# Kernel optimization log

Hardware: AMD Instinct MI355X
Metric: run time of the kernel (lower is better)

The kernel has to match this reference:

```python
import math
import jax, jax.numpy as jnp
import numpy as np

B, L, DIM, H = 2, 2048, 1024, 16
D = DIM // H  # head_dim = 64
EPS = 1e-6


def setup_inputs() -> dict:
    key = jax.random.key(0)
    ks = jax.random.split(key, 5)
    s = 0.02
    return {
        "x": jax.random.normal(ks[0], (B, L, DIM), jnp.float32),
        "pe": jax.random.normal(ks[1], (B, 1, L, D // 2, 2, 2), jnp.float32),
        "w_qkv": jax.random.normal(ks[2], (DIM, 3 * DIM), jnp.float32) * s,
        "q_scale": jnp.ones((D,), jnp.float32),
        "k_scale": jnp.ones((D,), jnp.float32),
        "w_proj": jax.random.normal(ks[3], (DIM, DIM), jnp.float32) * s,
        "b_proj": jnp.zeros((DIM,), jnp.float32),
    }


def _rmsnorm(t, scale):
    # flax nnx.RMSNorm: x * rsqrt(mean(x^2) + eps) * scale, over last dim
    var = jnp.mean(jnp.square(t), axis=-1, keepdims=True)
    return t * jax.lax.rsqrt(var + EPS) * scale


def _apply_rope(t, pe):
    # t: [B,H,L,D]; pe: [B,1,L,D/2,2,2]
    t2 = t.reshape(*t.shape[:-1], D // 2, 1, 2)
    out = pe[..., 0] * t2[..., 0] + pe[..., 1] * t2[..., 1]  # [B,H,L,D/2,2]
    return out.reshape(t.shape)


def reference(x, pe, w_qkv, q_scale, k_scale, w_proj, b_proj):
    # fused QKV projection
    qkv = jnp.einsum('bld,de->ble', x, w_qkv)  # [B,L,3*DIM]
    qkv = qkv.reshape(B, L, 3, H, D).transpose(2, 0, 3, 1, 4)  # [3,B,H,L,D]
    q, k, v = qkv[0], qkv[1], qkv[2]
    # QK RMSNorm
    q = _rmsnorm(q, q_scale)
    k = _rmsnorm(k, k_scale)
    # RoPE via pe
    q = _apply_rope(q, pe)
    k = _apply_rope(k, pe)
    # scaled dot product attention
    scores = jnp.einsum('bhqd,bhkd->bhqk', q, k) / math.sqrt(D)
    attn = jax.nn.softmax(scores, axis=-1)
    o = jnp.einsum('bhqk,bhkd->bhqd', attn, v)  # [B,H,L,D]
    o = o.transpose(0, 2, 1, 3).reshape(B, L, DIM)  # B H L D -> B L (H D)
    # output projection
    return jnp.einsum('bld,de->ble', o, w_proj) + b_proj
```

## Files before the change

kernel.cpp:

```cpp
#include <hip/hip_runtime.h>
#include <math.h>

#define BB 2
#define LL 2048
#define DIMM 1024
#define HH 16
#define DD 64
#define QKV_N 3072

typedef unsigned short u16;
typedef unsigned int u32;
typedef __attribute__((ext_vector_type(8))) short short8;
typedef __attribute__((ext_vector_type(4))) float f32x4;

__device__ __forceinline__ float bf2f(u16 h) {
    unsigned u = ((unsigned)h) << 16;
    return __uint_as_float(u);
}
__device__ __forceinline__ u16 f2bf(float f) {
    unsigned u = __float_as_uint(f);
    u += 0x7fffu + ((u >> 16) & 1u);
    return (u16)(u >> 16);
}
__device__ __forceinline__ u32 pack_bf2(float lo, float hi) {
    u32 a = __float_as_uint(hi) + 0x8000u;
    u32 b = __float_as_uint(lo) + 0x8000u;
    return __builtin_amdgcn_perm(a, b, 0x07060302u);
}
__device__ __forceinline__ void gload16(const u16* g, u16* l) {
    __builtin_amdgcn_global_load_lds(
        (const __attribute__((address_space(1))) void*)g,
        (__attribute__((address_space(3))) void*)l, 16, 0, 0);
}

__global__ __launch_bounds__(256) void convx(
    const float* __restrict__ X, u16* __restrict__ Xb)
{
    int i = (blockIdx.x * 256 + threadIdx.x) * 8;
    float4 a = *(const float4*)&X[i];
    float4 b = *(const float4*)&X[i + 4];
    u16 t[8] = {f2bf(a.x), f2bf(a.y), f2bf(a.z), f2bf(a.w),
                f2bf(b.x), f2bf(b.y), f2bf(b.z), f2bf(b.w)};
    *(uint4*)&Xb[i] = *(uint4*)t;
}

__global__ __launch_bounds__(256) void convt(
    const float* __restrict__ W, u16* __restrict__ Wt, int K, int N)
{
    __shared__ u16 s[64][72];
    const int tid = threadIdx.x;
    const int k0 = blockIdx.x * 64, n0 = blockIdx.y * 64;
#pragma unroll
    for (int t = 0; t < 16; ++t) {
        int flat = t * 256 + tid;
        int kk = flat >> 6, nn = flat & 63;
        s[nn][kk] = f2bf(W[(size_t)(k0 + kk) * N + n0 + nn]);
    }
    __syncthreads();
#pragma unroll
    for (int t = 0; t < 2; ++t) {
        int chunk = t * 256 + tid;
        int nn = chunk >> 3, kc = chunk & 7;
        *(uint4*)&Wt[(size_t)(n0 + nn) * K + k0 + kc * 8] = *(uint4*)&s[nn][kc * 8];
    }
}

__global__ __launch_bounds__(256) void gemm_qkv(
    const u16* __restrict__ A, const u16* __restrict__ Bt,
    u16* __restrict__ C, u16* __restrict__ vt, const float* __restrict__ pe,
    const float* __restrict__ qs, const float* __restrict__ ks)
{
    __shared__ u16 smem[2 * 128 * 64];
    u16* sA = smem;
    u16* sB = smem + 128 * 64;

    const int tid = threadIdx.x;
    const int wave = tid >> 6, lane = tid & 63;
    const int mIdx = lane & 15, quad = lane >> 4;
    const int wr = wave >> 1, wc = wave & 1;
    const int m0 = blockIdx.y * 128, n0 = blockIdx.x * 128;
    const int N = QKV_N, K = DIMM;
    const int lr = lane >> 3, lc = lane & 7;

    f32x4 acc[4][4];
#pragma unroll
    for (int a = 0; a < 4; ++a)
#pragma unroll
        for (int b = 0; b < 4; ++b) acc[a][b] = (f32x4){0.f, 0.f, 0.f, 0.f};

    for (int k0 = 0; k0 < K; k0 += 64) {
#pragma unroll
        for (int j = 0; j < 4; ++j) {
            int r0 = 32 * wave + 8 * j + lr;
            int kc = 8 * (lc ^ (r0 & 7));
            gload16(&A[(size_t)(m0 + r0) * K + k0 + kc], &sA[(32 * wave + 8 * j) * 64]);
            gload16(&Bt[(size_t)(n0 + r0) * K + k0 + kc], &sB[(32 * wave + 8 * j) * 64]);
        }
        __syncthreads();
#pragma unroll
        for (int ks2 = 0; ks2 < 2; ++ks2) {
            short8 af[4], bfr[4];
#pragma unroll
            for (int mt = 0; mt < 4; ++mt) {
                int Ra = 64 * wr + 16 * mt + mIdx;
                af[mt] = *(const short8*)&sA[Ra * 64 + 8 * ((ks2 * 4 + quad) ^ (Ra & 7))];
            }
#pragma unroll
            for (int nt = 0; nt < 4; ++nt) {
                int Rb = 64 * wc + 16 * nt + mIdx;
                bfr[nt] = *(const short8*)&sB[Rb * 64 + 8 * ((ks2 * 4 + quad) ^ (Rb & 7))];
            }
#pragma unroll
            for (int mt = 0; mt < 4; ++mt)
#pragma unroll
                for (int nt = 0; nt < 4; ++nt)
                    acc[mt][nt] = __builtin_amdgcn_mfma_f32_16x16x32_bf16(
                        af[mt], bfr[nt], acc[mt][nt], 0, 0, 0);
        }
        __syncthreads();
    }

    if (n0 >= 2048) {
#pragma unroll
        for (int mt = 0; mt < 4; ++mt) {
            int lofs = 64 * wr + 16 * mt + 4 * quad;
#pragma unroll
            for (int nt = 0; nt < 4; ++nt) {
                int d = 64 * wc + 16 * nt + mIdx;
                uint2 pr;
                pr.x = pack_bf2(acc[mt][nt][0], acc[mt][nt][1]);
                pr.y = pack_bf2(acc[mt][nt][2], acc[mt][nt][3]);
                *(uint2*)&smem[d * 128 + (lofs ^ (8 * (d & 7)))] = pr;
            }
        }
        __syncthreads();
        {
            const int d = tid >> 1, half = tid & 1;
            const int hd = n0 - 2048 + d;
            const int h = hd >> 6, dd = hd & 63;
            const int b = m0 >> 11, l0 = m0 & 2047;
            u16* dst = vt + ((size_t)((b * 16 + h) * 64 + dd)) * LL + l0 + half * 64;
#pragma unroll
            for (int c = 0; c < 8; ++c) {
                int slot = (half * 64 + 8 * c) ^ (8 * (d & 7));
                *(uint4*)&dst[8 * c] = *(const uint4*)&smem[d * 128 + slot];
            }
        }
    } else {
        const float* scv = (n0 < 1024) ? qs : ks;
        const float pre = (n0 < 1024) ? 0.18033688011112042f : 1.0f;
        float scl[4];
#pragma unroll
        for (int nt = 0; nt < 4; ++nt) scl[nt] = scv[16 * nt + mIdx];

#pragma unroll
        for (int mt = 0; mt < 4; ++mt) {
#pragma unroll
            for (int r = 0; r < 4; ++r) {
                float s = 0.f;
#pragma unroll
                for (int nt = 0; nt < 4; ++nt) {
                    float a = acc[mt][nt][r];
                    s += a * a;
                }
                s += __shfl_xor(s, 1);
                s += __shfl_xor(s, 2);
                s += __shfl_xor(s, 4);
                s += __shfl_xor(s, 8);
                float rn = rsqrtf(s * (1.f / 64.f) + 1e-6f);
                int R = m0 + 64 * wr + 16 * mt + quad * 4 + r;
                size_t peo = (size_t)R * 128;
#pragma unroll
                for (int nt = 0; nt < 4; ++nt) {
                    float v = acc[mt][nt][r] * rn * scl[nt];
                    float pp = __shfl_xor(v, 1);
                    float2 pw = *(const float2*)&pe[peo + 2 * (16 * nt + mIdx)];
                    float e  = (mIdx & 1) ? pp : v;
                    float od = (mIdx & 1) ? v : pp;
                    C[(size_t)R * N + n0 + 64 * wc + 16 * nt + mIdx] =
                        f2bf((pw.x * e + pw.y * od) * pre);
                }
            }
        }
    }
}

__global__ __launch_bounds__(256) void gemm_proj(
    const u16* __restrict__ A, const u16* __restrict__ Bt,
    const float* __restrict__ bias, float* __restrict__ C)
{
    __shared__ u16 sA[64 * 64];
    __shared__ u16 sB[128 * 64];

    const int tid = threadIdx.x;
    const int wave = tid >> 6, lane = tid & 63;
    const int mIdx = lane & 15, quad = lane >> 4;
    const int wr = wave >> 1, wc = wave & 1;
    const int m0 = blockIdx.y * 64, n0 = blockIdx.x * 128;
    const int N = DIMM, K = DIMM;
    const int lr = lane >> 3, lc = lane & 7;

    f32x4 acc[2][4];
#pragma unroll
    for (int a = 0; a < 2; ++a)
#pragma unroll
        for (int b = 0; b < 4; ++b) acc[a][b] = (f32x4){0.f, 0.f, 0.f, 0.f};

    for (int k0 = 0; k0 < K; k0 += 64) {
#pragma unroll
        for (int j = 0; j < 2; ++j) {
            int r0 = 16 * wave + 8 * j + lr;
            int kc = 8 * (lc ^ (r0 & 7));
            gload16(&A[(size_t)(m0 + r0) * K + k0 + kc], &sA[(16 * wave + 8 * j) * 64]);
        }
#pragma unroll
        for (int j = 0; j < 4; ++j) {
            int r0 = 32 * wave + 8 * j + lr;
            int kc = 8 * (lc ^ (r0 & 7));
            gload16(&Bt[(size_t)(n0 + r0) * K + k0 + kc], &sB[(32 * wave + 8 * j) * 64]);
        }
        __syncthreads();
#pragma unroll
        for (int ks2 = 0; ks2 < 2; ++ks2) {
            short8 af[2], bfr[4];
#pragma unroll
            for (int mt = 0; mt < 2; ++mt) {
                int Ra = 32 * wr + 16 * mt + mIdx;
                af[mt] = *(const short8*)&sA[Ra * 64 + 8 * ((ks2 * 4 + quad) ^ (Ra & 7))];
            }
#pragma unroll
            for (int nt = 0; nt < 4; ++nt) {
                int Rb = 64 * wc + 16 * nt + mIdx;
                bfr[nt] = *(const short8*)&sB[Rb * 64 + 8 * ((ks2 * 4 + quad) ^ (Rb & 7))];
            }
#pragma unroll
            for (int mt = 0; mt < 2; ++mt)
#pragma unroll
                for (int nt = 0; nt < 4; ++nt)
                    acc[mt][nt] = __builtin_amdgcn_mfma_f32_16x16x32_bf16(
                        af[mt], bfr[nt], acc[mt][nt], 0, 0, 0);
        }
        __syncthreads();
    }

#pragma unroll
    for (int mt = 0; mt < 2; ++mt)
#pragma unroll
        for (int r = 0; r < 4; ++r) {
            int row = m0 + 32 * wr + 16 * mt + quad * 4 + r;
#pragma unroll
            for (int nt = 0; nt < 4; ++nt) {
                int col = n0 + 64 * wc + 16 * nt + mIdx;
                C[(size_t)row * N + col] = acc[mt][nt][r] + bias[col];
            }
        }
}

#define PR 72

__global__ __launch_bounds__(512, 4) void attn_mfma(
    const u16* __restrict__ qkv, const u16* __restrict__ vt, u16* __restrict__ o)
{
    __shared__ u16 sK[2][64 * PR];
    __shared__ u16 sVt[2][64 * PR];
    __shared__ u16 sP[128 * PR];

    const int tid = threadIdx.x;
    const int wave = tid >> 6;
    const int lane = tid & 63;
    const int mIdx = lane & 15;
    const int quad = lane >> 4;

    const int bh = blockIdx.x >> 4;
    const int qt = blockIdx.x & 15;
    const int b = bh >> 4, h = bh & 15;
    const int q0 = qt * 128;

    const u16* kbase = qkv + (size_t)b * LL * QKV_N + 1024 + h * 64;
    const u16* vbase = vt + (size_t)bh * 64 * LL;

    const u16* qrow = qkv + (size_t)b * LL * QKV_N + h * 64
                      + (size_t)(q0 + 16 * wave + mIdx) * QKV_N;
    short8 aq0 = *(const short8*)&qrow[quad * 8];
    short8 aq1 = *(const short8*)&qrow[32 + quad * 8];

    const int sr = tid >> 3;
    const int sc = (tid & 7) * 8;

    {
        uint4 kv4 = *(const uint4*)&kbase[(size_t)sr * QKV_N + sc];
        uint4 vv4 = *(const uint4*)&vbase[(size_t)sr * LL + sc];
        *(uint4*)&sK[0][sr * PR + sc] = kv4;
        *(uint4*)&sVt[0][sr * PR + sc] = vv4;
    }

    float lsum = 0.f;
    f32x4 Oacc[4];
#pragma unroll
    for (int nb = 0; nb < 4; ++nb) Oacc[nb] = (f32x4){0.f, 0.f, 0.f, 0.f};

    u16* sProw = &sP[(16 * wave + mIdx) * PR];

    for (int kt = 0; kt < 32; ++kt) {
        const int p = kt & 1;
        __syncthreads();

        if (kt + 1 < 32) {
            const int k0n = (kt + 1) * 64;
            uint4 kv4 = *(const uint4*)&kbase[(size_t)(k0n + sr) * QKV_N + sc];
            uint4 vv4 = *(const uint4*)&vbase[(size_t)sr * LL + k0n + sc];
            *(uint4*)&sK[p ^ 1][sr * PR + sc] = kv4;
            *(uint4*)&sVt[p ^ 1][sr * PR + sc] = vv4;
        }

#pragma unroll
        for (int nb = 0; nb < 4; ++nb) {
            short8 bk0 = *(const short8*)&sK[p][(16 * nb + mIdx) * PR + quad * 8];
            short8 bk1 = *(const short8*)&sK[p][(16 * nb + mIdx) * PR + 32 + quad * 8];
            f32x4 st = (f32x4){0.f, 0.f, 0.f, 0.f};
            st = __builtin_amdgcn_mfma_f32_16x16x32_bf16(bk0, aq0, st, 0, 0, 0);
            st = __builtin_amdgcn_mfma_f32_16x16x32_bf16(bk1, aq1, st, 0, 0, 0);

            float p0 = exp2f(st[0]), p1 = exp2f(st[1]);
            float p2 = exp2f(st[2]), p3 = exp2f(st[3]);
            lsum += (p0 + p1) + (p2 + p3);
            u32 w0 = pack_bf2(p0, p1);
            u32 w1 = pack_bf2(p2, p3);
            uint2 wpair; wpair.x = w0; wpair.y = w1;
            *(uint2*)&sProw[16 * nb + quad * 4] = wpair;
        }

        short8 pa0 = *(const short8*)&sProw[quad * 8];
        short8 pa1 = *(const short8*)&sProw[32 + quad * 8];
#pragma unroll
        for (int nb = 0; nb < 4; ++nb) {
            short8 bv0 = *(const short8*)&sVt[p][(16 * nb + mIdx) * PR + quad * 8];
            short8 bv1 = *(const short8*)&sVt[p][(16 * nb + mIdx) * PR + 32 + quad * 8];
            Oacc[nb] = __builtin_amdgcn_mfma_f32_16x16x32_bf16(pa0, bv0, Oacc[nb], 0, 0, 0);
            Oacc[nb] = __builtin_amdgcn_mfma_f32_16x16x32_bf16(pa1, bv1, Oacc[nb], 0, 0, 0);
        }
    }

    lsum += __shfl_xor(lsum, 16);
    lsum += __shfl_xor(lsum, 32);

#pragma unroll
    for (int r = 0; r < 4; ++r) {
        float lr = __shfl(lsum, quad * 4 + r);
        float linv = 1.f / lr;
        int rowg = b * LL + q0 + 16 * wave + quad * 4 + r;
#pragma unroll
        for (int nb = 0; nb < 4; ++nb) {
            o[(size_t)rowg * DIMM + h * 64 + 16 * nb + mIdx] = f2bf(Oacc[nb][r] * linv);
        }
    }
}

extern "C" void kernel_launch(void* const* d_in, const int* in_sizes, int n_in,
                              void* d_out, int out_size, void* d_ws, size_t ws_size,
                              hipStream_t stream) {
    const float* x       = (const float*)d_in[0];
    const float* pe      = (const float*)d_in[1];
    const float* w_qkv   = (const float*)d_in[2];
    const float* q_scale = (const float*)d_in[3];
    const float* k_scale = (const float*)d_in[4];
    const float* w_proj  = (const float*)d_in[5];
    const float* b_proj  = (const float*)d_in[6];
    float* out = (float*)d_out;

    char* ws = (char*)d_ws;
    u16* qkv    = (u16*)ws;  ws += (size_t)4096 * 3072 * 2;
    u16* o      = (u16*)ws;  ws += (size_t)4096 * 1024 * 2;
    u16* xb     = (u16*)ws;  ws += (size_t)4096 * 1024 * 2;
    u16* wqkvt  = (u16*)ws;  ws += (size_t)3072 * 1024 * 2;
    u16* wprojt = (u16*)ws;  ws += (size_t)1024 * 1024 * 2;
    u16* vtbuf  = (u16*)ws;  ws += (size_t)BB * HH * DD * LL * 2;

    convx<<<(4096 * 1024) / (256 * 8), 256, 0, stream>>>(x, xb);
    convt<<<dim3(1024 / 64, QKV_N / 64), 256, 0, stream>>>(w_qkv, wqkvt, DIMM, QKV_N);
    convt<<<dim3(1024 / 64, 1024 / 64), 256, 0, stream>>>(w_proj, wprojt, DIMM, DIMM);

    gemm_qkv<<<dim3(QKV_N / 128, (BB * LL) / 128), 256, 0, stream>>>(
        xb, wqkvt, qkv, vtbuf, pe, q_scale, k_scale);

    attn_mfma<<<BB * HH * (LL / 128), 512, 0, stream>>>(qkv, vtbuf, o);

    gemm_proj<<<dim3(DIMM / 128, (BB * LL) / 64), 256, 0, stream>>>(
        o, wprojt, b_proj, out);
}
```

Baseline: 224.8 us.

## Restructure attention to 4 waves with 32 query rows each, swizzled LDS, async loads

The attention kernel now runs with 256 threads, and each wave handles 32 query rows (two 16-row groups), so every K/V fragment read from LDS feeds twice as many MFMAs. The padded LDS rows are replaced by an XOR-swizzled 64-wide layout, which avoids bank conflicts and cuts LDS footprint. Tile loads go through a gload16 direct global-to-LDS helper instead of register staging. The trade-off is more accumulator registers per thread and fewer waves per block to hide latency. gload16 is assumed to be defined in the part of the file not shown.

After: 222.6 us. About the same (-1.0%).

```diff
diff --git a/kernel.cpp b/kernel.cpp
--- a/kernel.cpp
+++ b/kernel.cpp
@@ -256,20 +256,19 @@
         }
 }
 
-#define PR 72
-
-__global__ __launch_bounds__(512, 4) void attn_mfma(
+__global__ __launch_bounds__(256, 2) void attn_mfma(
     const u16* __restrict__ qkv, const u16* __restrict__ vt, u16* __restrict__ o)
 {
-    __shared__ u16 sK[2][64 * PR];
-    __shared__ u16 sVt[2][64 * PR];
-    __shared__ u16 sP[128 * PR];
+    __shared__ u16 sK[2][64 * 64];
+    __shared__ u16 sVt[2][64 * 64];
+    __shared__ u16 sP[128 * 64];
 
     const int tid = threadIdx.x;
     const int wave = tid >> 6;
     const int lane = tid & 63;
     const int mIdx = lane & 15;
     const int quad = lane >> 4;
+    const int m7 = mIdx & 7;
 
     const int bh = blockIdx.x >> 4;
     const int qt = blockIdx.x & 15;
@@ -279,27 +278,36 @@
     const u16* kbase = qkv + (size_t)b * LL * QKV_N + 1024 + h * 64;
     const u16* vbase = vt + (size_t)bh * 64 * LL;
 
-    const u16* qrow = qkv + (size_t)b * LL * QKV_N + h * 64
-                      + (size_t)(q0 + 16 * wave + mIdx) * QKV_N;
-    short8 aq0 = *(const short8*)&qrow[quad * 8];
-    short8 aq1 = *(const short8*)&qrow[32 + quad * 8];
-
-    const int sr = tid >> 3;
-    const int sc = (tid & 7) * 8;
-
-    {
-        uint4 kv4 = *(const uint4*)&kbase[(size_t)sr * QKV_N + sc];
-        uint4 vv4 = *(const uint4*)&vbase[(size_t)sr * LL + sc];
-        *(uint4*)&sK[0][sr * PR + sc] = kv4;
-        *(uint4*)&sVt[0][sr * PR + sc] = vv4;
-    }
-
-    float lsum = 0.f;
-    f32x4 Oacc[4];
-#pragma unroll
-    for (int nb = 0; nb < 4; ++nb) Oacc[nb] = (f32x4){0.f, 0.f, 0.f, 0.f};
-
-    u16* sProw = &sP[(16 * wave + mIdx) * PR];
+    short8 aq[2][2];
+#pragma unroll
+    for (int g = 0; g < 2; ++g) {
+        const u16* qrow = qkv + (size_t)b * LL * QKV_N + h * 64
+                          + (size_t)(q0 + 32 * wave + 16 * g + mIdx) * QKV_N;
+        aq[g][0] = *(const short8*)&qrow[quad * 8];
+        aq[g][1] = *(const short8*)&qrow[32 + quad * 8];
+    }
+
+    const int lr = lane >> 3, lc = lane & 7;
+    const int sw = 8 * (lc ^ lr);
+
+#pragma unroll
+    for (int i = 0; i < 2; ++i) {
+        const int row = 16 * wave + 8 * i + lr;
+        gload16(&kbase[(size_t)row * QKV_N + sw], &sK[0][(16 * wave + 8 * i) * 64]);
+        gload16(&vbase[(size_t)row * LL + sw], &sVt[0][(16 * wave + 8 * i) * 64]);
+    }
+
+    float lsum[2] = {0.f, 0.f};
+    f32x4 Oacc[2][4];
+#pragma unroll
+    for (int g = 0; g < 2; ++g)
+#pragma unroll
+        for (int nb = 0; nb < 4; ++nb) Oacc[g][nb] = (f32x4){0.f, 0.f, 0.f, 0.f};
+
+    const int o0 = 8 * (quad ^ m7);
+    const int o1 = 8 * ((quad + 4) ^ m7);
+    u16* sPr0 = &sP[(32 * wave + mIdx) * 64];
+    u16* sPr1 = &sP[(32 * wave + 16 + mIdx) * 64];
 
     for (int kt = 0; kt < 32; ++kt) {
         const int p = kt & 1;
@@ -307,51 +315,68 @@
 
         if (kt + 1 < 32) {
             const int k0n = (kt + 1) * 64;
-            uint4 kv4 = *(const uint4*)&kbase[(size_t)(k0n + sr) * QKV_N + sc];
-            uint4 vv4 = *(const uint4*)&vbase[(size_t)sr * LL + k0n + sc];
-            *(uint4*)&sK[p ^ 1][sr * PR + sc] = kv4;
-            *(uint4*)&sVt[p ^ 1][sr * PR + sc] = vv4;
+#pragma unroll
+            for (int i = 0; i < 2; ++i) {
+                const int row = 16 * wave + 8 * i + lr;
+                gload16(&kbase[(size_t)(k0n + row) * QKV_N + sw],
+                        &sK[p ^ 1][(16 * wave + 8 * i) * 64]);
+                gload16(&vbase[(size_t)row * LL + k0n + sw],
+                        &sVt[p ^ 1][(16 * wave + 8 * i) * 64]);
+            }
         }
 
 #pragma unroll
         for (int nb = 0; nb < 4; ++nb) {
-            short8 bk0 = *(const short8*)&sK[p][(16 * nb + mIdx) * PR + quad * 8];
-            short8 bk1 = *(const short8*)&sK[p][(16 * nb + mIdx) * PR + 32 + quad * 8];
-            f32x4 st = (f32x4){0.f, 0.f, 0.f, 0.f};
-            st = __builtin_amdgcn_mfma_f32_16x16x32_bf16(bk0, aq0, st, 0, 0, 0);
-            st = __builtin_amdgcn_mfma_f32_16x16x32_bf16(bk1, aq1, st, 0, 0, 0);
-
-            float p0 = exp2f(st[0]), p1 = exp2f(st[1]);
-            float p2 = exp2f(st[2]), p3 = exp2f(st[3]);
-            lsum += (p0 + p1) + (p2 + p3);
-            u32 w0 = pack_bf2(p0, p1);
-            u32 w1 = pack_bf2(p2, p3);
-            uint2 wpair; wpair.x = w0; wpair.y = w1;
-            *(uint2*)&sProw[16 * nb + quad * 4] = wpair;
-        }
-
-        short8 pa0 = *(const short8*)&sProw[quad * 8];
-        short8 pa1 = *(const short8*)&sProw[32 + quad * 8];
+            const u16* krow = &sK[p][(16 * nb + mIdx) * 64];
+            short8 bk0 = *(const short8*)&krow[o0];
+            short8 bk1 = *(const short8*)&krow[o1];
+            const int pofs = (16 * nb + 4 * quad) ^ (8 * m7);
+#pragma unroll
+            for (int g = 0; g < 2; ++g) {
+                f32x4 st = (f32x4){0.f, 0.f, 0.f, 0.f};
+                st = __builtin_amdgcn_mfma_f32_16x16x32_bf16(bk0, aq[g][0], st, 0, 0, 0);
+                st = __builtin_amdgcn_mfma_f32_16x16x32_bf16(bk1, aq[g][1], st, 0, 0, 0);
+                float p0 = exp2f(st[0]), p1 = exp2f(st[1]);
+                float p2 = exp2f(st[2]), p3 = exp2f(st[3]);
+                lsum[g] += (p0 + p1) + (p2 + p3);
+                uint2 wp;
+                wp.x = pack_bf2(p0, p1);
+                wp.y = pack_bf2(p2, p3);
+                *(uint2*)&((g == 0 ? sPr0 : sPr1)[pofs]) = wp;
+            }
+        }
+
+        short8 pa00 = *(const short8*)&sPr0[o0];
+        short8 pa01 = *(const short8*)&sPr0[o1];
+        short8 pa10 = *(const short8*)&sPr1[o0];
+        short8 pa11 = *(const short8*)&sPr1[o1];
 #pragma unroll
         for (int nb = 0; nb < 4; ++nb) {
-            short8 bv0 = *(const short8*)&sVt[p][(16 * nb + mIdx) * PR + quad * 8];
-            short8 bv1 = *(const short8*)&sVt[p][(16 * nb + mIdx) * PR + 32 + quad * 8];
-            Oacc[nb] = __builtin_amdgcn_mfma_f32_16x16x32_bf16(pa0, bv0, Oacc[nb], 0, 0, 0);
-            Oacc[nb] = __builtin_amdgcn_mfma_f32_16x16x32_bf16(pa1, bv1, Oacc[nb], 0, 0, 0);
-        }
-    }
-
-    lsum += __shfl_xor(lsum, 16);
-    lsum += __shfl_xor(lsum, 32);
-
-#pragma unroll
-    for (int r = 0; r < 4; ++r) {
-        float lr = __shfl(lsum, quad * 4 + r);
-        float linv = 1.f / lr;
-        int rowg = b * LL + q0 + 16 * wave + quad * 4 + r;
-#pragma unroll
-        for (int nb = 0; nb < 4; ++nb) {
-            o[(size_t)rowg * DIMM + h * 64 + 16 * nb + mIdx] = f2bf(Oacc[nb][r] * linv);
+            const u16* vrow = &sVt[p][(16 * nb + mIdx) * 64];
+            short8 bv0 = *(const short8*)&vrow[o0];
+            short8 bv1 = *(const short8*)&vrow[o1];
+            Oacc[0][nb] = __builtin_amdgcn_mfma_f32_16x16x32_bf16(pa00, bv0, Oacc[0][nb], 0, 0, 0);
+            Oacc[0][nb] = __builtin_amdgcn_mfma_f32_16x16x32_bf16(pa01, bv1, Oacc[0][nb], 0, 0, 0);
+            Oacc[1][nb] = __builtin_amdgcn_mfma_f32_16x16x32_bf16(pa10, bv0, Oacc[1][nb], 0, 0, 0);
+            Oacc[1][nb] = __builtin_amdgcn_mfma_f32_16x16x32_bf16(pa11, bv1, Oacc[1][nb], 0, 0, 0);
+        }
+    }
+
+#pragma unroll
+    for (int g = 0; g < 2; ++g) {
+        float ls = lsum[g];
+        ls += __shfl_xor(ls, 16);
+        ls += __shfl_xor(ls, 32);
+#pragma unroll
+        for (int r = 0; r < 4; ++r) {
+            float lv = __shfl(ls, quad * 4 + r);
+            float linv = 1.f / lv;
+            const int rowg = b * LL + q0 + 32 * wave + 16 * g + quad * 4 + r;
+#pragma unroll
+            for (int nb = 0; nb < 4; ++nb) {
+                o[(size_t)rowg * DIMM + h * 64 + 16 * nb + mIdx] =
+                    f2bf(Oacc[g][nb][r] * linv);
+            }
         }
     }
 }
@@ -383,7 +408,7 @@
     gemm_qkv<<<dim3(QKV_N / 128, (BB * LL) / 128), 256, 0, stream>>>(
         xb, wqkvt, qkv, vtbuf, pe, q_scale, k_scale);
 
-    attn_mfma<<<BB * HH * (LL / 128), 512, 0, stream>>>(qkv, vtbuf, o);
+    attn_mfma<<<BB * HH * (LL / 128), 256, 0, stream>>>(qkv, vtbuf, o);
 
     gemm_proj<<<dim3(DIMM / 128, (BB * LL) / 64), 256, 0, stream>>>(
         o, wprojt, b_proj, out);
```
